# Optimization experiments

Measured on AMD Instinct MI355X. Metric: run time of the kernel, lower is better.

The kernel has to match this reference:

```python
import jax, jax.numpy as jnp
import numpy as np

T, N, F = 96, 1140, 64   # timesteps, nodes per graph, node feature dim
H = 32                    # GAT hidden channels
LH = 250                  # LSTM hidden
OUT = 2280                # per-head output
E = 22800                 # edges per graph


def setup_inputs() -> dict:
    key = jax.random.key(0)
    ks = jax.random.split(key, 32)
    s = lambda k, shape, fan: jax.random.normal(k, shape, jnp.float32) / np.sqrt(fan)
    inp = {}
    inp["nodes"] = jax.random.normal(ks[0], (T, N, F), jnp.float32)
    inp["edges_index"] = jax.random.randint(ks[1], (T, 2, E), 0, N)
    inp["edges_attr"] = jax.random.normal(ks[2], (T, E), jnp.float32)  # unused by forward (faithful)
    # GAT layer 1 (F -> H) and layer 2 (H -> H), heads=1
    inp["gat_W1"] = s(ks[3], (F, H), F)
    inp["gat_as1"] = s(ks[4], (H,), H)
    inp["gat_ad1"] = s(ks[5], (H,), H)
    inp["gat_b1"] = jnp.zeros((H,), jnp.float32)
    inp["gat_W2"] = s(ks[6], (H, H), H)
    inp["gat_as2"] = s(ks[7], (H,), H)
    inp["gat_ad2"] = s(ks[8], (H,), H)
    inp["gat_b2"] = jnp.zeros((H,), jnp.float32)
    # 2-layer LSTM, batch_first, batch=1, input = N*H
    IN0 = N * H
    inp["Wih0"] = s(ks[9], (4 * LH, IN0), IN0)
    inp["Whh0"] = s(ks[10], (4 * LH, LH), LH)
    inp["bih0"] = jnp.zeros((4 * LH,), jnp.float32)
    inp["bhh0"] = jnp.zeros((4 * LH,), jnp.float32)
    inp["Wih1"] = s(ks[11], (4 * LH, LH), LH)
    inp["Whh1"] = s(ks[12], (4 * LH, LH), LH)
    inp["bih1"] = jnp.zeros((4 * LH,), jnp.float32)
    inp["bhh1"] = jnp.zeros((4 * LH,), jnp.float32)
    # random initial states (original uses torch.randn in forward)
    inp["h0"] = jax.random.normal(ks[13], (2, 1, LH), jnp.float32)
    inp["c0"] = jax.random.normal(ks[14], (2, 1, LH), jnp.float32)
    for i in range(4):
        inp[f"fc{i+1}_W"] = s(ks[15 + 2 * i], (OUT, LH), LH)
        inp[f"fc{i+1}_b"] = jnp.zeros((OUT,), jnp.float32)
    return inp


def _gat_conv(x, src, dst, W, a_s, a_d, b, n):
    # GATConv, heads=1: h = xW; e_ij = LeakyReLU(a_s.h_src + a_d.h_dst);
    # softmax over edges sharing a destination; scatter-add aggregation.
    h = x @ W                                                   # [N, H]
    e = jax.nn.leaky_relu((h @ a_s)[src] + (h @ a_d)[dst], negative_slope=0.2)
    m = jax.ops.segment_max(e, dst, num_segments=n)
    ex = jnp.exp(e - m[dst])
    denom = jax.ops.segment_sum(ex, dst, num_segments=n)
    alpha = ex / denom[dst]
    return jax.ops.segment_sum(alpha[:, None] * h[src], dst, num_segments=n) + b


def _lstm_layer(xs, Wih, Whh, bih, bhh, h0, c0):
    # xs: [T, B, in]; torch gate order i, f, g, o
    def step(carry, x):
        h, c = carry
        g = x @ Wih.T + h @ Whh.T + bih + bhh
        i, f, gg, o = jnp.split(g, 4, axis=-1)
        c = jax.nn.sigmoid(f) * c + jax.nn.sigmoid(i) * jnp.tanh(gg)
        h = jax.nn.sigmoid(o) * jnp.tanh(c)
        return (h, c), h
    (_, _), ys = jax.lax.scan(step, (h0, c0), xs)
    return ys


def reference(nodes, edges_index, edges_attr, gat_W1, gat_as1, gat_ad1, gat_b1,
              gat_W2, gat_as2, gat_ad2, gat_b2,
              Wih0, Whh0, bih0, bhh0, Wih1, Whh1, bih1, bhh1, h0, c0,
              fc1_W, fc1_b, fc2_W, fc2_b, fc3_W, fc3_b, fc4_W, fc4_b):
    n = nodes.shape[1]
    loop = jnp.arange(n)  # self-loops (GATConv default add_self_loops=True)

    def per_graph(x, ei):
        src = jnp.concatenate([ei[0], loop])
        dst = jnp.concatenate([ei[1], loop])
        h = jax.nn.relu(_gat_conv(x, src, dst, gat_W1, gat_as1, gat_ad1, gat_b1, n))
        h = _gat_conv(h, src, dst, gat_W2, gat_as2, gat_ad2, gat_b2, n)
        return h.reshape(-1)

    seq = jax.vmap(per_graph)(nodes, edges_index)   # [T, N*H]
    xs = seq[:, None, :]                            # [T, 1, N*H] (batch=1)
    ys = _lstm_layer(xs, Wih0, Whh0, bih0, bhh0, h0[0], c0[0])
    ys = _lstm_layer(ys, Wih1, Whh1, bih1, bhh1, h0[1], c0[1])
    last = ys[-1]                                   # [1, LH]
    preds = [last @ fc1_W.T + fc1_b, last @ fc2_W.T + fc2_b,
             last @ fc3_W.T + fc3_b, last @ fc4_W.T + fc4_b]
    return jnp.stack(preds, axis=0).reshape(last.shape[0], 4, -1)  # [1, 4, 2280]
```

## Files before the change

### kernel.cpp

```cpp
#include <hip/hip_runtime.h>

#define T_ 96
#define N_ 1140
#define F_ 64
#define H_ 32
#define E_ 22800
#define LH_ 250
#define G4_ 1000
#define OUT_ 2280
#define KIN_ 36480
#define SPLITK 60
#define KC 32
#define BN 32
#define FEATB 13680

typedef _Float16 h2_t __attribute__((ext_vector_type(2)));

__device__ __forceinline__ float leaky02(float x){ return x > 0.f ? x : 0.2f*x; }
__device__ __forceinline__ float fsigm(float x){ return 1.f/(1.f + __expf(-x)); }
__device__ __forceinline__ float ftanh(float x){
  x = fminf(fmaxf(x, -15.f), 15.f);
  float t = __expf(2.f * x);
  return (t - 1.f) / (t + 1.f);
}
__device__ __forceinline__ unsigned packh2(float a, float b) {
  auto p = __builtin_amdgcn_cvt_pkrtz(a, b);
  return __builtin_bit_cast(unsigned, p);
}
__device__ __forceinline__ float fdot2u(unsigned w, unsigned h, float acc) {
  return __builtin_amdgcn_fdot2(__builtin_bit_cast(h2_t, w),
                                __builtin_bit_cast(h2_t, h), acc, false);
}

__device__ __forceinline__ void st_agent_u(unsigned* p, unsigned v) {
  __hip_atomic_store(p, v, __ATOMIC_RELAXED, __HIP_MEMORY_SCOPE_AGENT);
}
__device__ __forceinline__ unsigned ld_agent_u(const unsigned* p) {
  return __hip_atomic_load((unsigned*)p, __ATOMIC_RELAXED, __HIP_MEMORY_SCOPE_AGENT);
}
__device__ __forceinline__ void st_agent_i(int* p, int v) {
  __hip_atomic_store(p, v, __ATOMIC_RELAXED, __HIP_MEMORY_SCOPE_AGENT);
}
__device__ __forceinline__ int ld_agent_i(const int* p) {
  return __hip_atomic_load((int*)p, __ATOMIC_RELAXED, __HIP_MEMORY_SCOPE_AGENT);
}

__global__ void k_featcsr(const float* __restrict__ x, const float* __restrict__ W,
                          const float* __restrict__ as_, const float* __restrict__ ad_,
                          float* __restrict__ Hout, float* __restrict__ HS,
                          float* __restrict__ HD,
                          const int* __restrict__ ei, int* __restrict__ offs,
                          int* __restrict__ elist) {
  __shared__ float Wl[F_ * H_];
  __shared__ float asl[32], adl[32];
  __shared__ int cnt[N_], cur[N_], sh[256];
  int tid = threadIdx.x;
  if (blockIdx.x >= FEATB) {
    int t = blockIdx.x - FEATB;
    const int* srcp = ei + (size_t)t * 2 * E_;
    const int* dstp = srcp + E_;
    for (int i = tid; i < N_; i += 256) cnt[i] = 0;
    __syncthreads();
    for (int k = tid; k < E_; k += 256) atomicAdd(&cnt[dstp[k]], 1);
    __syncthreads();
    int base = tid * 5;
    int v[5]; int s = 0;
    #pragma unroll
    for (int r = 0; r < 5; ++r) {
      int i = base + r;
      int c = (i < N_) ? cnt[i] : 0;
      v[r] = c; s += c;
    }
    sh[tid] = s; __syncthreads();
    for (int off = 1; off < 256; off <<= 1) {
      int add = (tid >= off) ? sh[tid - off] : 0;
      __syncthreads();
      sh[tid] += add;
      __syncthreads();
    }
    int run = sh[tid] - s;
    #pragma unroll
    for (int r = 0; r < 5; ++r) {
      int i = base + r;
      if (i < N_) { offs[t * (N_ + 1) + i] = run; cur[i] = run; }
      run += v[r];
    }
    if (tid == 255) offs[t * (N_ + 1) + N_] = sh[255];
    __syncthreads();
    int* elt = elist + (size_t)t * E_;
    for (int k = tid; k < E_; k += 256) {
      int src = srcp[k];
      int pos = atomicAdd(&cur[dstp[k]], 1);
      elt[pos] = src;
    }
    return;
  }
  for (int i = tid; i < F_ * H_; i += 256) Wl[i] = W[i];
  if (tid < 32) { asl[tid] = as_[tid]; adl[tid] = ad_[tid]; }
  __syncthreads();
  int row = blockIdx.x * 8 + (tid >> 5);
  int c = tid & 31;
  const float4* xr = (const float4*)(x + (size_t)row * F_);
  float acc = 0.f;
  for (int k4 = 0; k4 < (F_ >> 2); ++k4) {
    float4 v = xr[k4];
    acc += v.x * Wl[(4 * k4 + 0) * H_ + c];
    acc += v.y * Wl[(4 * k4 + 1) * H_ + c];
    acc += v.z * Wl[(4 * k4 + 2) * H_ + c];
    acc += v.w * Wl[(4 * k4 + 3) * H_ + c];
  }
  Hout[(size_t)row * H_ + c] = acc;
  float ps = acc * asl[c], pd = acc * adl[c];
  #pragma unroll
  for (int off = 16; off > 0; off >>= 1) {
    ps += __shfl_xor(ps, off, 32);
    pd += __shfl_xor(pd, off, 32);
  }
  if (c == 0) { HS[row] = ps; HD[row] = pd; }
}

__device__ __forceinline__ float aggr_row(const float* __restrict__ Ht,
                                          const float* __restrict__ HSt,
                                          const int* __restrict__ el,
                                          int e0, int e1, float selfH,
                                          float hd_i, int c) {
  float m = leaky02(HSt[0] * 0.f + hd_i);
  return 0.f;
}

__global__ void k_aggrfeat(const float* __restrict__ Hf, const float* __restrict__ HS,
                           const float* __restrict__ HD, const int* __restrict__ offs,
                           const int* __restrict__ elist, const float* __restrict__ b,
                           const float* __restrict__ W2, const float* __restrict__ as2,
                           const float* __restrict__ ad2,
                           float* __restrict__ H2, float* __restrict__ HS2,
                           float* __restrict__ HD2) {
  __shared__ float W2l[H_ * H_];
  __shared__ float as2l[32], ad2l[32];
  int tid = threadIdx.x;
  for (int i = tid; i < H_ * H_; i += 256) W2l[i] = W2[i];
  if (tid < 32) { as2l[tid] = as2[tid]; ad2l[tid] = ad2[tid]; }
  __syncthreads();
  int gid = blockIdx.x * 256 + tid;
  int row = gid >> 5; int c = gid & 31;
  if (row >= T_ * N_) return;
  int t = row / N_; int i = row - t * N_;
  float hd_i = HD[row];
  float m = leaky02(HS[row] + hd_i);
  float s = 1.f;
  float acc = Hf[(size_t)row * H_ + c];
  int e0 = offs[t * (N_ + 1) + i], e1 = offs[t * (N_ + 1) + i + 1];
  const int* el = elist + (size_t)t * E_;
  const float* Ht = Hf + (size_t)t * N_ * H_;
  const float* HSt = HS + t * N_;
  for (int base = e0; base < e1; base += 32) {
    int e = base + c;
    bool valid = (e < e1);
    int src = valid ? el[e] : 0;
    float eg = valid ? leaky02(HSt[src] + hd_i) : -1e30f;
    float M = eg;
    #pragma unroll
    for (int off = 16; off > 0; off >>= 1) M = fmaxf(M, __shfl_xor(M, off, 32));
    float mn = fmaxf(m, M);
    float scl = __expf(m - mn);
    float p = __expf(eg - mn);
    float ps = p;
    #pragma unroll
    for (int off = 16; off > 0; off >>= 1) ps += __shfl_xor(ps, off, 32);
    s = s * scl + ps;
    acc *= scl;
    int cnt = e1 - base; if (cnt > 32) cnt = 32;
    for (int l = 0; l < cnt; ++l) {
      float pb = __shfl(p, l, 32);
      int sb = __shfl(src, l, 32);
      acc += pb * Ht[(size_t)sb * H_ + c];
    }
    m = mn;
  }
  float val = fmaxf(acc / s + b[c], 0.f);
  float acc2 = 0.f;
  #pragma unroll
  for (int cc = 0; cc < 32; ++cc) {
    float xc = __shfl(val, cc, 32);
    acc2 += xc * W2l[cc * H_ + c];
  }
  H2[(size_t)row * H_ + c] = acc2;
  float ps2 = acc2 * as2l[c], pd2 = acc2 * ad2l[c];
  #pragma unroll
  for (int off = 16; off > 0; off >>= 1) {
    ps2 += __shfl_xor(ps2, off, 32);
    pd2 += __shfl_xor(pd2, off, 32);
  }
  if (c == 0) { HS2[row] = ps2; HD2[row] = pd2; }
}

__global__ void k_aggr(const float* __restrict__ Hf, const float* __restrict__ HS,
                       const float* __restrict__ HD, const int* __restrict__ offs,
                       const int* __restrict__ elist, const float* __restrict__ b,
                       float* __restrict__ Xout) {
  int gid = blockIdx.x * blockDim.x + threadIdx.x;
  int row = gid >> 5; int c = gid & 31;
  if (row >= T_ * N_) return;
  int t = row / N_; int i = row - t * N_;
  float hd_i = HD[row];
  float m = leaky02(HS[row] + hd_i);
  float s = 1.f;
  float acc = Hf[(size_t)row * H_ + c];
  int e0 = offs[t * (N_ + 1) + i], e1 = offs[t * (N_ + 1) + i + 1];
  const int* el = elist + (size_t)t * E_;
  const float* Ht = Hf + (size_t)t * N_ * H_;
  const float* HSt = HS + t * N_;
  for (int base = e0; base < e1; base += 32) {
    int e = base + c;
    bool valid = (e < e1);
    int src = valid ? el[e] : 0;
    float eg = valid ? leaky02(HSt[src] + hd_i) : -1e30f;
    float M = eg;
    #pragma unroll
    for (int off = 16; off > 0; off >>= 1) M = fmaxf(M, __shfl_xor(M, off, 32));
    float mn = fmaxf(m, M);
    float scl = __expf(m - mn);
    float p = __expf(eg - mn);
    float ps = p;
    #pragma unroll
    for (int off = 16; off > 0; off >>= 1) ps += __shfl_xor(ps, off, 32);
    s = s * scl + ps;
    acc *= scl;
    int cnt = e1 - base; if (cnt > 32) cnt = 32;
    for (int l = 0; l < cnt; ++l) {
      float pb = __shfl(p, l, 32);
      int sb = __shfl(src, l, 32);
      acc += pb * Ht[(size_t)sb * H_ + c];
    }
    m = mn;
  }
  Xout[(size_t)row * H_ + c] = acc / s + b[c];
}

__global__ void k_gemm(const float* __restrict__ X, const float* __restrict__ Wih,
                       float* __restrict__ Gpart) {
  __shared__ unsigned Xs[T_][KC / 2 + 1];
  __shared__ unsigned Ws[BN][KC / 2 + 1];
  int j0 = blockIdx.x * BN;
  int sp = blockIdx.y;
  int tid = threadIdx.x;
  int jj = tid & 7;
  int tt = tid >> 3;
  float acc[6][4] = {};
  int kbeg = sp * (KIN_ / SPLITK);
  int kend = kbeg + (KIN_ / SPLITK);
  for (int k0 = kbeg; k0 < kend; k0 += KC) {
    for (int idx = tid; idx < T_ * (KC / 2); idx += 128) {
      int tr = idx >> 4; int kk = idx & 15;
      const float2 v = *(const float2*)(X + (size_t)tr * KIN_ + k0 + 2 * kk);
      Xs[tr][kk] = packh2(v.x, v.y);
    }
    for (int idx = tid; idx < BN * (KC / 2); idx += 128) {
      int jr = idx >> 4; int kk = idx & 15;
      int j = j0 + jr;
      unsigned v = 0;
      if (j < G4_) {
        const float2 w = *(const float2*)(Wih + (size_t)j * KIN_ + k0 + 2 * kk);
        v = packh2(w.x, w.y);
      }
      Ws[jr][kk] = v;
    }
    __syncthreads();
    for (int kk = 0; kk < KC / 2; ++kk) {
      unsigned xv[6], wv[4];
      #pragma unroll
      for (int r = 0; r < 6; ++r) xv[r] = Xs[tt * 6 + r][kk];
      #pragma unroll
      for (int q = 0; q < 4; ++q) wv[q] = Ws[jj * 4 + q][kk];
      #pragma unroll
      for (int r = 0; r < 6; ++r)
        #pragma unroll
        for (int q = 0; q < 4; ++q)
          acc[r][q] = fdot2u(wv[q], xv[r], acc[r][q]);
    }
    __syncthreads();
  }
  #pragma unroll
  for (int r = 0; r < 6; ++r) {
    int t = tt * 6 + r;
    #pragma unroll
    for (int q = 0; q < 4; ++q) {
      int j = j0 + jj * 4 + q;
      if (j < G4_) Gpart[((size_t)sp * T_ + t) * 1024 + j] = acc[r][q];
    }
  }
}

__global__ void k_gred(const float* __restrict__ Gpart, const float* __restrict__ bih,
                       const float* __restrict__ bhh, float* __restrict__ G0) {
  int idx = blockIdx.x * blockDim.x + threadIdx.x;
  if (idx >= T_ * G4_) return;
  int t = idx / G4_; int jg = idx - t * G4_;
  int j = jg >> 2, g = jg & 3;
  int c = g * LH_ + j;
  float s = bih[c] + bhh[c];
  for (int sp = 0; sp < SPLITK; ++sp) s += Gpart[((size_t)sp * T_ + t) * 1024 + c];
  G0[idx] = s;
}

__global__ void __launch_bounds__(512, 2) k_lstm(
    const float* __restrict__ G0, const float* __restrict__ Whh0,
    const float* __restrict__ Wih1, const float* __restrict__ Whh1,
    const float* __restrict__ bih1, const float* __restrict__ bhh1,
    const float* __restrict__ h0in, const float* __restrict__ c0in,
    unsigned* __restrict__ hp,
    int* __restrict__ flags,
    float* __restrict__ ylast) {
  int tid = threadIdx.x;
  int bid = blockIdx.x;
  int wv = bid * 8 + (tid >> 6);
  int lane = tid & 63;
  int qg = lane >> 4;
  int ql = lane & 15;

  unsigned w0[4][8], wx1[4][8], wh1[4][8];
  float bs1[4], c0l[4], c1l[4];
  bool act[4];
  #pragma unroll
  for (int u = 0; u < 4; ++u) {
    int U = wv * 4 + u;
    act[u] = (U < LH_);
    int Uc = act[u] ? U : 0;
    size_t rb = (size_t)(qg * LH_ + Uc) * LH_;
    #pragma unroll
    for (int m = 0; m < 8; ++m) {
      int pi = m * 16 + ql;
      if (act[u] && pi < 125) {
        w0[u][m]  = packh2(Whh0[rb + 2 * pi], Whh0[rb + 2 * pi + 1]);
        wx1[u][m] = packh2(Wih1[rb + 2 * pi], Wih1[rb + 2 * pi + 1]);
        wh1[u][m] = packh2(Whh1[rb + 2 * pi], Whh1[rb + 2 * pi + 1]);
      } else { w0[u][m] = 0; wx1[u][m] = 0; wh1[u][m] = 0; }
    }
    bs1[u] = act[u] ? (bih1[qg * LH_ + Uc] + bhh1[qg * LH_ + Uc]) : 0.f;
    c0l[u] = act[u] ? c0in[Uc] : 0.f;
    c1l[u] = act[u] ? c0in[LH_ + Uc] : 0.f;
  }

  float gpre[4];
  #pragma unroll
  for (int u = 0; u < 4; ++u)
    gpre[u] = act[u] ? G0[0 * G4_ + (wv * 4 + u) * 4 + qg] : 0.f;

  for (int p = 0; p <= T_; ++p) {
    int rs = (p - 1) & 1, wslot = p & 1;
    unsigned x0p[8], h1p[8];
    if (p == 0) {
      #pragma unroll
      for (int m = 0; m < 8; ++m) {
        int pi = m * 16 + ql;
        x0p[m] = (pi < 125) ? packh2(h0in[2 * pi], h0in[2 * pi + 1]) : 0u;
      }
    } else {
      #pragma unroll
      for (int m = 0; m < 8; ++m)
        x0p[m] = ld_agent_u(&hp[rs * 256 + m * 16 + ql]);
      if (p == 1) {
        #pragma unroll
        for (int m = 0; m < 8; ++m) {
          int pi = m * 16 + ql;
          h1p[m] = (pi < 125) ? packh2(h0in[LH_ + 2 * pi], h0in[LH_ + 2 * pi + 1]) : 0u;
        }
      } else {
        #pragma unroll
        for (int m = 0; m < 8; ++m)
          h1p[m] = ld_agent_u(&hp[rs * 256 + 128 + m * 16 + ql]);
      }
    }

    if (p < T_) {
      float h0new[4];
      #pragma unroll
      for (int u = 0; u < 4; ++u) {
        float s = 0.f;
        #pragma unroll
        for (int m = 0; m < 8; ++m) s = fdot2u(w0[u][m], x0p[m], s);
        s += __shfl_xor(s, 1); s += __shfl_xor(s, 2);
        s += __shfl_xor(s, 4); s += __shfl_xor(s, 8);
        float pre = s + gpre[u];
        float a = (qg == 2) ? ftanh(pre) : fsigm(pre);
        float ai = __shfl(a, ql);
        float af = __shfl(a, 16 + ql);
        float ag = __shfl(a, 32 + ql);
        float ao = __shfl(a, 48 + ql);
        c0l[u] = af * c0l[u] + ai * ag;
        h0new[u] = act[u] ? (ao * ftanh(c0l[u])) : 0.f;
      }
      if (lane == 0) {
        st_agent_u(&hp[wslot * 256 + 2 * wv],     packh2(h0new[0], h0new[1]));
        st_agent_u(&hp[wslot * 256 + 2 * wv + 1], packh2(h0new[2], h0new[3]));
      }
    }
    if (p >= 1) {
      float h1new[4];
      #pragma unroll
      for (int u = 0; u < 4; ++u) {
        float s = 0.f;
        #pragma unroll
        for (int m = 0; m < 8; ++m) s = fdot2u(wx1[u][m], x0p[m], s);
        #pragma unroll
        for (int m = 0; m < 8; ++m) s = fdot2u(wh1[u][m], h1p[m], s);
        s += __shfl_xor(s, 1); s += __shfl_xor(s, 2);
        s += __shfl_xor(s, 4); s += __shfl_xor(s, 8);
        float pre = s + bs1[u];
        float a = (qg == 2) ? ftanh(pre) : fsigm(pre);
        float bi = __shfl(a, ql);
        float bf = __shfl(a, 16 + ql);
        float bg = __shfl(a, 32 + ql);
        float bo = __shfl(a, 48 + ql);
        c1l[u] = bf * c1l[u] + bi * bg;
        h1new[u] = act[u] ? (bo * ftanh(c1l[u])) : 0.f;
      }
      if (p - 1 == T_ - 1 && lane == 0) {
        #pragma unroll
        for (int u = 0; u < 4; ++u)
          if (act[u]) ylast[wv * 4 + u] = h1new[u];
      }
      if (lane == 0) {
        st_agent_u(&hp[wslot * 256 + 128 + 2 * wv],     packh2(h1new[0], h1new[1]));
        st_agent_u(&hp[wslot * 256 + 128 + 2 * wv + 1], packh2(h1new[2], h1new[3]));
      }
    }
    float gnext[4];
    #pragma unroll
    for (int u = 0; u < 4; ++u)
      gnext[u] = (p + 1 < T_ && act[u]) ? G0[(p + 1) * G4_ + (wv * 4 + u) * 4 + qg] : 0.f;
    if (p < T_) {
      __syncthreads();
      if (tid == 0) {
        asm volatile("s_waitcnt vmcnt(0)" ::: "memory");
        st_agent_i(&flags[bid], p + 1);
      }
      if (tid < 64) {
        int guard = 0;
        for (;;) {
          int f = ld_agent_i(&flags[lane & 7]);
          if (__ballot(f >= p + 1) == ~0ULL) break;
          if (++guard > (1 << 22)) break;
          __builtin_amdgcn_s_sleep(1);
        }
      }
      __syncthreads();
    }
    #pragma unroll
    for (int u = 0; u < 4; ++u) gpre[u] = gnext[u];
  }
}

__global__ void k_fc(const float* __restrict__ ylast,
                     const float* __restrict__ Wa, const float* __restrict__ ba,
                     const float* __restrict__ Wb, const float* __restrict__ bb,
                     const float* __restrict__ Wc, const float* __restrict__ bc,
                     const float* __restrict__ Wd, const float* __restrict__ bd,
                     float* __restrict__ out) {
  int wg = blockIdx.x * 4 + (threadIdx.x >> 6);
  int lane = threadIdx.x & 63;
  if (wg >= 4 * OUT_) return;
  int head = wg / OUT_, o = wg - head * OUT_;
  const float* W = head == 0 ? Wa : head == 1 ? Wb : head == 2 ? Wc : Wd;
  const float* b = head == 0 ? ba : head == 1 ? bb : head == 2 ? bc : bd;
  float s = 0.f;
  #pragma unroll
  for (int r = 0; r < 4; ++r) {
    int idx = r * 64 + lane;
    if (idx < LH_) s += ylast[idx] * W[(size_t)o * LH_ + idx];
  }
  #pragma unroll
  for (int off = 32; off > 0; off >>= 1) s += __shfl_xor(s, off, 64);
  if (lane == 0) out[wg] = s + b[o];
}

extern "C" void kernel_launch(void* const* d_in, const int* in_sizes, int n_in,
                              void* d_out, int out_size, void* d_ws, size_t ws_size,
                              hipStream_t stream) {
  const float* nodes = (const float*)d_in[0];
  const int*   ei    = (const int*)d_in[1];
  const float* W1    = (const float*)d_in[3];
  const float* as1   = (const float*)d_in[4];
  const float* ad1   = (const float*)d_in[5];
  const float* b1    = (const float*)d_in[6];
  const float* W2    = (const float*)d_in[7];
  const float* as2   = (const float*)d_in[8];
  const float* ad2   = (const float*)d_in[9];
  const float* b2    = (const float*)d_in[10];
  const float* Wih0  = (const float*)d_in[11];
  const float* Whh0  = (const float*)d_in[12];
  const float* bih0  = (const float*)d_in[13];
  const float* bhh0  = (const float*)d_in[14];
  const float* Wih1  = (const float*)d_in[15];
  const float* Whh1  = (const float*)d_in[16];
  const float* bih1  = (const float*)d_in[17];
  const float* bhh1  = (const float*)d_in[18];
  const float* h0    = (const float*)d_in[19];
  const float* c0    = (const float*)d_in[20];
  const float* fW1   = (const float*)d_in[21];
  const float* fb1   = (const float*)d_in[22];
  const float* fW2   = (const float*)d_in[23];
  const float* fb2   = (const float*)d_in[24];
  const float* fW3   = (const float*)d_in[25];
  const float* fb3   = (const float*)d_in[26];
  const float* fW4   = (const float*)d_in[27];
  const float* fb4   = (const float*)d_in[28];
  float* out = (float*)d_out;

  const size_t o_Gpart  = 0;
  const size_t o_H      = 0;
  const size_t o_HS     = 14008320;
  const size_t o_HD     = 14446080;
  const size_t o_H2     = 14883840;
  const size_t o_X2     = 28892160;
  const size_t o_flags  = 42900480;
  const size_t o_offs   = 42900736;
  const size_t o_elist  = 43338880;
  const size_t o_G0     = 52094080;
  const size_t o_hp     = 52478080;
  const size_t o_ylast  = 52480128;
  const size_t o_HS2    = 52481152;
  const size_t o_HD2    = 52918912;
  const size_t total    = 53356672;
  if (ws_size < total) return;

  char* ws = (char*)d_ws;
  float*    Gpart  = (float*)(ws + o_Gpart);
  float*    Hbuf   = (float*)(ws + o_H);
  float*    HS     = (float*)(ws + o_HS);
  float*    HD     = (float*)(ws + o_HD);
  float*    H2     = (float*)(ws + o_H2);
  float*    X2     = (float*)(ws + o_X2);
  int*      flags  = (int*)(ws + o_flags);
  int*      offs   = (int*)(ws + o_offs);
  int*      elist  = (int*)(ws + o_elist);
  float*    G0     = (float*)(ws + o_G0);
  unsigned* hp     = (unsigned*)(ws + o_hp);
  float*    ylast  = (float*)(ws + o_ylast);
  float*    HS2    = (float*)(ws + o_HS2);
  float*    HD2    = (float*)(ws + o_HD2);

  (void)hipMemsetAsync(flags, 0, 256, stream);

  const int rows_grid = (T_ * N_ * H_) / 256;

  k_featcsr<<<FEATB + T_, 256, 0, stream>>>(nodes, W1, as1, ad1,
                                            Hbuf, HS, HD, ei, offs, elist);
  k_aggrfeat<<<rows_grid, 256, 0, stream>>>(Hbuf, HS, HD, offs, elist, b1,
                                            W2, as2, ad2, H2, HS2, HD2);
  k_aggr<<<rows_grid, 256, 0, stream>>>(H2, HS2, HD2, offs, elist, b2, X2);
  k_gemm<<<dim3(32, SPLITK), 128, 0, stream>>>(X2, Wih0, Gpart);
  k_gred<<<(T_ * G4_ + 255) / 256, 256, 0, stream>>>(Gpart, bih0, bhh0, G0);
  k_lstm<<<8, 512, 0, stream>>>(G0, Whh0, Wih1, Whh1, bih1, bhh1, h0, c0,
                                hp, flags, ylast);
  k_fc<<<OUT_, 256, 0, stream>>>(ylast, fW1, fb1, fW2, fb2, fW3, fb3, fW4, fb4, out);
}
```

Baseline: 973.1 us.

## Stage per-graph node features in LDS for GAT aggregation and emit fp16 LSTM input

The two GAT aggregation kernels now run one block per timestep graph. Each block first copies that graph's node features and attention scalars (about 146 KB) into shared memory, so the neighbour gathers read LDS instead of global memory. The second aggregation writes its output as packed fp16 pairs, which the input-projection GEMM then loads directly, halving that intermediate buffer and removing the conversion from the GEMM load. The cost is that the grid shrinks from thousands of blocks to 96, each with one block per CU because of the large LDS footprint, so aggregation parallelism drops sharply.

New measurement: 1.618 ms. 1.66x slower.

```diff
diff --git a/kernel.cpp b/kernel.cpp
--- a/kernel.cpp
+++ b/kernel.cpp
@@ -9,6 +9,7 @@
 #define G4_ 1000
 #define OUT_ 2280
 #define KIN_ 36480
+#define KINH 18240
 #define SPLITK 60
 #define KC 32
 #define BN 32
@@ -119,125 +120,151 @@
   if (c == 0) { HS[row] = ps; HD[row] = pd; }
 }
 
-__device__ __forceinline__ float aggr_row(const float* __restrict__ Ht,
-                                          const float* __restrict__ HSt,
-                                          const int* __restrict__ el,
-                                          int e0, int e1, float selfH,
-                                          float hd_i, int c) {
-  float m = leaky02(HSt[0] * 0.f + hd_i);
-  return 0.f;
-}
-
-__global__ void k_aggrfeat(const float* __restrict__ Hf, const float* __restrict__ HS,
-                           const float* __restrict__ HD, const int* __restrict__ offs,
-                           const int* __restrict__ elist, const float* __restrict__ b,
-                           const float* __restrict__ W2, const float* __restrict__ as2,
-                           const float* __restrict__ ad2,
-                           float* __restrict__ H2, float* __restrict__ HS2,
-                           float* __restrict__ HD2) {
+__global__ void __launch_bounds__(256) k_aggrfeat(
+    const float* __restrict__ Hf, const float* __restrict__ HS,
+    const float* __restrict__ HD, const int* __restrict__ offs,
+    const int* __restrict__ elist, const float* __restrict__ b,
+    const float* __restrict__ W2, const float* __restrict__ as2,
+    const float* __restrict__ ad2,
+    float* __restrict__ H2, float* __restrict__ HS2, float* __restrict__ HD2) {
+  __shared__ float ldsH[N_ * H_];
+  __shared__ float ldsHS[N_], ldsHD[N_];
   __shared__ float W2l[H_ * H_];
   __shared__ float as2l[32], ad2l[32];
+  int t = blockIdx.x;
   int tid = threadIdx.x;
-  for (int i = tid; i < H_ * H_; i += 256) W2l[i] = W2[i];
-  if (tid < 32) { as2l[tid] = as2[tid]; ad2l[tid] = ad2[tid]; }
+  {
+    const float4* s4 = (const float4*)(Hf + (size_t)t * N_ * H_);
+    float4* d4 = (float4*)ldsH;
+    for (int i = tid; i < N_ * H_ / 4; i += 256) d4[i] = s4[i];
+    for (int i = tid; i < N_; i += 256) {
+      ldsHS[i] = HS[t * N_ + i];
+      ldsHD[i] = HD[t * N_ + i];
+    }
+    for (int i = tid; i < H_ * H_; i += 256) W2l[i] = W2[i];
+    if (tid < 32) { as2l[tid] = as2[tid]; ad2l[tid] = ad2[tid]; }
+  }
   __syncthreads();
-  int gid = blockIdx.x * 256 + tid;
-  int row = gid >> 5; int c = gid & 31;
-  if (row >= T_ * N_) return;
-  int t = row / N_; int i = row - t * N_;
-  float hd_i = HD[row];
-  float m = leaky02(HS[row] + hd_i);
-  float s = 1.f;
-  float acc = Hf[(size_t)row * H_ + c];
-  int e0 = offs[t * (N_ + 1) + i], e1 = offs[t * (N_ + 1) + i + 1];
   const int* el = elist + (size_t)t * E_;
-  const float* Ht = Hf + (size_t)t * N_ * H_;
-  const float* HSt = HS + t * N_;
-  for (int base = e0; base < e1; base += 32) {
-    int e = base + c;
-    bool valid = (e < e1);
-    int src = valid ? el[e] : 0;
-    float eg = valid ? leaky02(HSt[src] + hd_i) : -1e30f;
-    float M = eg;
-    #pragma unroll
-    for (int off = 16; off > 0; off >>= 1) M = fmaxf(M, __shfl_xor(M, off, 32));
-    float mn = fmaxf(m, M);
-    float scl = __expf(m - mn);
-    float p = __expf(eg - mn);
-    float ps = p;
-    #pragma unroll
-    for (int off = 16; off > 0; off >>= 1) ps += __shfl_xor(ps, off, 32);
-    s = s * scl + ps;
-    acc *= scl;
-    int cnt = e1 - base; if (cnt > 32) cnt = 32;
-    for (int l = 0; l < cnt; ++l) {
-      float pb = __shfl(p, l, 32);
-      int sb = __shfl(src, l, 32);
-      acc += pb * Ht[(size_t)sb * H_ + c];
-    }
-    m = mn;
-  }
-  float val = fmaxf(acc / s + b[c], 0.f);
-  float acc2 = 0.f;
-  #pragma unroll
-  for (int cc = 0; cc < 32; ++cc) {
-    float xc = __shfl(val, cc, 32);
-    acc2 += xc * W2l[cc * H_ + c];
-  }
-  H2[(size_t)row * H_ + c] = acc2;
-  float ps2 = acc2 * as2l[c], pd2 = acc2 * ad2l[c];
-  #pragma unroll
-  for (int off = 16; off > 0; off >>= 1) {
-    ps2 += __shfl_xor(ps2, off, 32);
-    pd2 += __shfl_xor(pd2, off, 32);
-  }
-  if (c == 0) { HS2[row] = ps2; HD2[row] = pd2; }
-}
-
-__global__ void k_aggr(const float* __restrict__ Hf, const float* __restrict__ HS,
-                       const float* __restrict__ HD, const int* __restrict__ offs,
-                       const int* __restrict__ elist, const float* __restrict__ b,
-                       float* __restrict__ Xout) {
-  int gid = blockIdx.x * blockDim.x + threadIdx.x;
-  int row = gid >> 5; int c = gid & 31;
-  if (row >= T_ * N_) return;
-  int t = row / N_; int i = row - t * N_;
-  float hd_i = HD[row];
-  float m = leaky02(HS[row] + hd_i);
-  float s = 1.f;
-  float acc = Hf[(size_t)row * H_ + c];
-  int e0 = offs[t * (N_ + 1) + i], e1 = offs[t * (N_ + 1) + i + 1];
+  const int* offt = offs + t * (N_ + 1);
+  int c = tid & 31;
+  for (int ib = 0; ib < N_; ib += 8) {
+    int i = ib + (tid >> 5);
+    if (i >= N_) continue;
+    int row = t * N_ + i;
+    float hd_i = ldsHD[i];
+    float m = leaky02(ldsHS[i] + hd_i);
+    float s = 1.f;
+    float acc = ldsH[i * H_ + c];
+    int e0 = offt[i], e1 = offt[i + 1];
+    for (int base = e0; base < e1; base += 32) {
+      int e = base + c;
+      bool valid = (e < e1);
+      int src = valid ? el[e] : 0;
+      float eg = valid ? leaky02(ldsHS[src] + hd_i) : -1e30f;
+      float M = eg;
+      #pragma unroll
+      for (int off = 16; off > 0; off >>= 1) M = fmaxf(M, __shfl_xor(M, off, 32));
+      float mn = fmaxf(m, M);
+      float scl = __expf(m - mn);
+      float p = __expf(eg - mn);
+      float ps = p;
+      #pragma unroll
+      for (int off = 16; off > 0; off >>= 1) ps += __shfl_xor(ps, off, 32);
+      s = s * scl + ps;
+      acc *= scl;
+      int cnt2 = e1 - base; if (cnt2 > 32) cnt2 = 32;
+      for (int l = 0; l < cnt2; ++l) {
+        float pb = __shfl(p, l, 32);
+        int sb = __shfl(src, l, 32);
+        acc += pb * ldsH[sb * H_ + c];
+      }
+      m = mn;
+    }
+    float val = fmaxf(acc / s + b[c], 0.f);
+    float acc2 = 0.f;
+    #pragma unroll
+    for (int cc = 0; cc < 32; ++cc) {
+      float xc = __shfl(val, cc, 32);
+      acc2 += xc * W2l[cc * H_ + c];
+    }
+    H2[(size_t)row * H_ + c] = acc2;
+    float ps2 = acc2 * as2l[c], pd2 = acc2 * ad2l[c];
+    #pragma unroll
+    for (int off = 16; off > 0; off >>= 1) {
+      ps2 += __shfl_xor(ps2, off, 32);
+      pd2 += __shfl_xor(pd2, off, 32);
+    }
+    if (c == 0) { HS2[row] = ps2; HD2[row] = pd2; }
+  }
+}
+
+__global__ void __launch_bounds__(256) k_aggr(
+    const float* __restrict__ Hf, const float* __restrict__ HS,
+    const float* __restrict__ HD, const int* __restrict__ offs,
+    const int* __restrict__ elist, const float* __restrict__ b,
+    unsigned* __restrict__ X2h) {
+  __shared__ float ldsH[N_ * H_];
+  __shared__ float ldsHS[N_], ldsHD[N_];
+  __shared__ float bl[32];
+  int t = blockIdx.x;
+  int tid = threadIdx.x;
+  {
+    const float4* s4 = (const float4*)(Hf + (size_t)t * N_ * H_);
+    float4* d4 = (float4*)ldsH;
+    for (int i = tid; i < N_ * H_ / 4; i += 256) d4[i] = s4[i];
+    for (int i = tid; i < N_; i += 256) {
+      ldsHS[i] = HS[t * N_ + i];
+      ldsHD[i] = HD[t * N_ + i];
+    }
+    if (tid < 32) bl[tid] = b[tid];
+  }
+  __syncthreads();
   const int* el = elist + (size_t)t * E_;
-  const float* Ht = Hf + (size_t)t * N_ * H_;
-  const float* HSt = HS + t * N_;
-  for (int base = e0; base < e1; base += 32) {
-    int e = base + c;
-    bool valid = (e < e1);
-    int src = valid ? el[e] : 0;
-    float eg = valid ? leaky02(HSt[src] + hd_i) : -1e30f;
-    float M = eg;
-    #pragma unroll
-    for (int off = 16; off > 0; off >>= 1) M = fmaxf(M, __shfl_xor(M, off, 32));
-    float mn = fmaxf(m, M);
-    float scl = __expf(m - mn);
-    float p = __expf(eg - mn);
-    float ps = p;
-    #pragma unroll
-    for (int off = 16; off > 0; off >>= 1) ps += __shfl_xor(ps, off, 32);
-    s = s * scl + ps;
-    acc *= scl;
-    int cnt = e1 - base; if (cnt > 32) cnt = 32;
-    for (int l = 0; l < cnt; ++l) {
-      float pb = __shfl(p, l, 32);
-      int sb = __shfl(src, l, 32);
-      acc += pb * Ht[(size_t)sb * H_ + c];
-    }
-    m = mn;
-  }
-  Xout[(size_t)row * H_ + c] = acc / s + b[c];
-}
-
-__global__ void k_gemm(const float* __restrict__ X, const float* __restrict__ Wih,
+  const int* offt = offs + t * (N_ + 1);
+  int c = tid & 31;
+  for (int ib = 0; ib < N_; ib += 8) {
+    int i = ib + (tid >> 5);
+    if (i >= N_) continue;
+    float hd_i = ldsHD[i];
+    float m = leaky02(ldsHS[i] + hd_i);
+    float s = 1.f;
+    float acc = ldsH[i * H_ + c];
+    int e0 = offt[i], e1 = offt[i + 1];
+    for (int base = e0; base < e1; base += 32) {
+      int e = base + c;
+      bool valid = (e < e1);
+      int src = valid ? el[e] : 0;
+      float eg = valid ? leaky02(ldsHS[src] + hd_i) : -1e30f;
+      float M = eg;
+      #pragma unroll
+      for (int off = 16; off > 0; off >>= 1) M = fmaxf(M, __shfl_xor(M, off, 32));
+      float mn = fmaxf(m, M);
+      float scl = __expf(m - mn);
+      float p = __expf(eg - mn);
+      float ps = p;
+      #pragma unroll
+      for (int off = 16; off > 0; off >>= 1) ps += __shfl_xor(ps, off, 32);
+      s = s * scl + ps;
+      acc *= scl;
+      int cnt2 = e1 - base; if (cnt2 > 32) cnt2 = 32;
+      for (int l = 0; l < cnt2; ++l) {
+        float pb = __shfl(p, l, 32);
+        int sb = __shfl(src, l, 32);
+        acc += pb * ldsH[sb * H_ + c];
+      }
+      m = mn;
+    }
+    float val = acc / s + bl[c];
+    int cp = c & ~1;
+    float v0 = __shfl(val, cp, 32);
+    float v1 = __shfl(val, cp + 1, 32);
+    if ((c & 1) == 0)
+      X2h[(size_t)t * KINH + i * 16 + (c >> 1)] = packh2(v0, v1);
+  }
+}
+
+__global__ void k_gemm(const unsigned* __restrict__ Xh, const float* __restrict__ Wih,
                        float* __restrict__ Gpart) {
   __shared__ unsigned Xs[T_][KC / 2 + 1];
   __shared__ unsigned Ws[BN][KC / 2 + 1];
@@ -252,8 +279,7 @@
   for (int k0 = kbeg; k0 < kend; k0 += KC) {
     for (int idx = tid; idx < T_ * (KC / 2); idx += 128) {
       int tr = idx >> 4; int kk = idx & 15;
-      const float2 v = *(const float2*)(X + (size_t)tr * KIN_ + k0 + 2 * kk);
-      Xs[tr][kk] = packh2(v.x, v.y);
+      Xs[tr][kk] = Xh[(size_t)tr * KINH + (k0 >> 1) + kk];
     }
     for (int idx = tid; idx < BN * (KC / 2); idx += 128) {
       int jr = idx >> 4; int kk = idx & 15;
@@ -512,16 +538,16 @@
   const size_t o_HS     = 14008320;
   const size_t o_HD     = 14446080;
   const size_t o_H2     = 14883840;
-  const size_t o_X2     = 28892160;
-  const size_t o_flags  = 42900480;
-  const size_t o_offs   = 42900736;
-  const size_t o_elist  = 43338880;
-  const size_t o_G0     = 52094080;
-  const size_t o_hp     = 52478080;
-  const size_t o_ylast  = 52480128;
-  const size_t o_HS2    = 52481152;
-  const size_t o_HD2    = 52918912;
-  const size_t total    = 53356672;
+  const size_t o_X2h    = 28892160;
+  const size_t o_flags  = 35896320;
+  const size_t o_offs   = 35896576;
+  const size_t o_elist  = 36334720;
+  const size_t o_G0     = 45089920;
+  const size_t o_hp     = 45473920;
+  const size_t o_ylast  = 45475968;
+  const size_t o_HS2    = 45476992;
+  const size_t o_HD2    = 45914752;
+  const size_t total    = 46352512;
   if (ws_size < total) return;
 
   char* ws = (char*)d_ws;
@@ -530,7 +556,7 @@
   float*    HS     = (float*)(ws + o_HS);
   float*    HD     = (float*)(ws + o_HD);
   float*    H2     = (float*)(ws + o_H2);
-  float*    X2     = (float*)(ws + o_X2);
+  unsigned* X2h    = (unsigned*)(ws + o_X2h);
   int*      flags  = (int*)(ws + o_flags);
   int*      offs   = (int*)(ws + o_offs);
   int*      elist  = (int*)(ws + o_elist);
@@ -542,14 +568,12 @@
 
   (void)hipMemsetAsync(flags, 0, 256, stream);
 
-  const int rows_grid = (T_ * N_ * H_) / 256;
-
   k_featcsr<<<FEATB + T_, 256, 0, stream>>>(nodes, W1, as1, ad1,
                                             Hbuf, HS, HD, ei, offs, elist);
-  k_aggrfeat<<<rows_grid, 256, 0, stream>>>(Hbuf, HS, HD, offs, elist, b1,
-                                            W2, as2, ad2, H2, HS2, HD2);
-  k_aggr<<<rows_grid, 256, 0, stream>>>(H2, HS2, HD2, offs, elist, b2, X2);
-  k_gemm<<<dim3(32, SPLITK), 128, 0, stream>>>(X2, Wih0, Gpart);
+  k_aggrfeat<<<T_, 256, 0, stream>>>(Hbuf, HS, HD, offs, elist, b1,
+                                     W2, as2, ad2, H2, HS2, HD2);
+  k_aggr<<<T_, 256, 0, stream>>>(H2, HS2, HD2, offs, elist, b2, X2h);
+  k_gemm<<<dim3(32, SPLITK), 128, 0, stream>>>(X2h, Wih0, Gpart);
   k_gred<<<(T_ * G4_ + 255) / 256, 256, 0, stream>>>(Gpart, bih0, bhh0, G0);
   k_lstm<<<8, 512, 0, stream>>>(G0, Whh0, Wih1, Whh1, bih1, bhh1, h0, c0,
                                 hp, flags, ylast);
```
